# Performance work log

Measured on AMD Instinct MI355X. Metric: run time of the kernel, lower is better.

The kernel has to match this reference:

```python
import jax, jax.numpy as jnp
import numpy as np

D = 256        # embedding_dim
N = 32768      # number of latent vectors (tokens)
K = 8192       # num_embeddings (codebook size)


def setup_inputs() -> dict:
    key = jax.random.key(0)
    k1, k2 = jax.random.split(key)
    z_e = jax.random.normal(k1, (D, N), dtype=jnp.float32)
    embeddings = jax.random.normal(k2, (K, D), dtype=jnp.float32)
    return {"z_e": z_e, "embeddings": embeddings}


def reference(z_e, embeddings):
    # z_e: (D, N), embeddings: (K, D)
    z = z_e.T  # (N, D)
    # squared euclidean distance via expansion ||z||^2 - 2 z.e + ||e||^2
    # (mathematically identical to sum((emb - z)**2, -1), avoids (N,K,D) temp)
    z_sq = jnp.sum(z * z, axis=1, keepdims=True)            # (N, 1)
    e_sq = jnp.sum(embeddings * embeddings, axis=1)         # (K,)
    dist = z_sq - 2.0 * (z @ embeddings.T) + e_sq[None, :]  # (N, K)
    indices = jnp.argmin(dist, axis=-1)                     # (N,)
    z_q = embeddings[indices].T                             # (D, N)
    return z_q, indices
```

## Files before the change

kernel.cpp:

```cpp
#include <hip/hip_runtime.h>

#define D_DIM 256
#define N_TOK 32768
#define K_CB  8192
#define TAU   0.12f
#define ZC_CAP 4096
#define SLABS 32
#define SLABW 256

typedef float    f32x16 __attribute__((ext_vector_type(16)));
typedef float    f32x4  __attribute__((ext_vector_type(4)));
typedef _Float16 f16x8  __attribute__((ext_vector_type(8)));

#define OFF_ESQ   0
#define OFF_CNT   32768
#define OFF_GDONE 33024
#define OFF_LIST  35072
#define OFF_FIXB  166144
#define OFF_EHT   524288
#define OFF_ZC    (OFF_EHT + 4194304)
#define OFF_PBV   (OFF_ZC + 4194304)
#define OFF_PSC   (OFF_PBV + 262144)
#define OFF_PBK   (OFF_PSC + 262144)
#define MAXGRP    512
#define WS_NEED   ((size_t)(OFF_PBK + 262144))

#define SMEM_MAIN 65536

__global__ __launch_bounds__(256) void eprep_kernel(const float* __restrict__ e,
                                                    short* __restrict__ eht,
                                                    float* __restrict__ esq,
                                                    int* __restrict__ cnt,
                                                    int* __restrict__ gdone) {
  __shared__ float ps[4 * 64];
  const int tid = threadIdx.x;
  const int kk = tid & 63, cc = tid >> 6;
  const int k = blockIdx.x * 64 + kk;
  if (blockIdx.x == 0) {
    if (tid == 0) *cnt = 0;
    if (tid < 256) { gdone[tid] = 0; gdone[tid + 256] = 0; }
  }
  _Float16* ef = (_Float16*)eht;
  float ss = 0.f;
  #pragma unroll
  for (int c2 = 0; c2 < 8; ++c2) {
    const int c = cc * 8 + c2;
    f32x4 v0 = *(const f32x4*)(e + (size_t)k * D_DIM + c * 8);
    f32x4 v1 = *(const f32x4*)(e + (size_t)k * D_DIM + c * 8 + 4);
    float v[8] = {v0[0], v0[1], v0[2], v0[3], v1[0], v1[1], v1[2], v1[3]};
    f16x8 hv;
    #pragma unroll
    for (int i = 0; i < 8; ++i) {
      ss += v[i] * v[i];
      hv[i] = (_Float16)v[i];
    }
    *(f16x8*)(ef + ((size_t)c * K_CB + k) * 8) = hv;
  }
  ps[cc * 64 + kk] = ss;
  __syncthreads();
  if (tid < 64)
    esq[blockIdx.x * 64 + tid] = ps[tid] + ps[64 + tid] + ps[128 + tid] + ps[192 + tid];
}

__global__ __launch_bounds__(512, 4) void vq_main_kernel(
    const float* __restrict__ z, const float* __restrict__ esq_g,
    const short* __restrict__ eht,
    float* __restrict__ pbv, float* __restrict__ psc, int* __restrict__ pbk) {
  extern __shared__ char smem[];
  _Float16* zs = (_Float16*)smem;

  const int tid  = threadIdx.x;
  const int w    = tid >> 6;
  const int lane = tid & 63;
  const int half = lane >> 5;
  const int l31  = lane & 31;
  const int tg   = blockIdx.x >> 1;
  const int kh   = blockIdx.x & 1;
  const int n0   = tg * 128;
  const _Float16* ef = (const _Float16*)eht;

  {
    const int t  = tid & 127;
    const int cb = (tid >> 7) * 8;
    #pragma unroll
    for (int cc = 0; cc < 8; ++cc) {
      const int c = cb + cc;
      f16x8 hv;
      #pragma unroll
      for (int i = 0; i < 8; ++i)
        hv[i] = (_Float16)(-2.0f * z[(size_t)(c * 8 + i) * N_TOK + n0 + t]);
      *(f16x8*)(zs + ((size_t)c * 128 + t) * 8) = hv;
    }
  }
  __syncthreads();

  float bestv[4] = {3.4e38f, 3.4e38f, 3.4e38f, 3.4e38f};
  float secv[4]  = {3.4e38f, 3.4e38f, 3.4e38f, 3.4e38f};
  int   bestk[4] = {0, 0, 0, 0};

  const int kbase = kh * (K_CB / 2);
  for (int k0 = 0; k0 < K_CB / 2; k0 += 256) {
    const int kb = kbase + k0 + w * 32;

    f32x16 acc[4];
    {
      const int qb = kb + 4 * half;
      #pragma unroll
      for (int g = 0; g < 4; ++g) {
        f32x4 q = *(const f32x4*)(esq_g + qb + 8 * g);
        #pragma unroll
        for (int r = 0; r < 4; ++r) {
          const float qv = q[r];
          #pragma unroll
          for (int j = 0; j < 4; ++j) acc[j][g * 4 + r] = qv;
        }
      }
    }

    #pragma unroll 1
    for (int dc = 0; dc < 16; ++dc) {
      f16x8 a, b[4];
      a = *(const f16x8*)(ef + ((size_t)(2 * dc + half) * K_CB + kb + l31) * 8);
      const int zb = ((2 * dc + half) * 128 + l31) * 8;
      #pragma unroll
      for (int j = 0; j < 4; ++j)
        b[j] = *(const f16x8*)(zs + zb + j * 32 * 8);
      #pragma unroll
      for (int j = 0; j < 4; ++j)
        acc[j] = __builtin_amdgcn_mfma_f32_32x32x16_f16(a, b[j], acc[j], 0, 0, 0);
    }

    {
      const int base = kb + 4 * half;
      #pragma unroll
      for (int g = 0; g < 4; ++g) {
        #pragma unroll
        for (int r = 0; r < 4; ++r) {
          const int reg = g * 4 + r;
          const int kglob = base + 8 * g + r;
          #pragma unroll
          for (int j = 0; j < 4; ++j) {
            const float s = acc[j][reg];
            if (s < bestv[j]) { secv[j] = bestv[j]; bestv[j] = s; bestk[j] = kglob; }
            else if (s < secv[j]) secv[j] = s;
          }
        }
      }
    }
  }

  __syncthreads();
  float* pv  = (float*)(smem);
  int*   pk  = (int*)  (smem + 8192);
  float* ps2 = (float*)(smem + 16384);
  const int slot = w * 2 + half;
  #pragma unroll
  for (int j = 0; j < 4; ++j) {
    const int t = j * 32 + l31;
    pv [slot * 128 + t] = bestv[j];
    pk [slot * 128 + t] = bestk[j];
    ps2[slot * 128 + t] = secv[j];
  }
  __syncthreads();
  if (tid < 128) {
    const int t = tid;
    float bv = pv[t]; int bk = pk[t]; float sc = ps2[t];
    #pragma unroll
    for (int s2 = 1; s2 < 16; ++s2) {
      float v = pv[s2 * 128 + t]; int k2 = pk[s2 * 128 + t]; float s3 = ps2[s2 * 128 + t];
      if (v < bv || (v == bv && k2 < bk)) { sc = fminf(bv, s3); bv = v; bk = k2; }
      else                                { sc = fminf(sc, v); }
    }
    const size_t o = ((size_t)kh * 256 + tg) * 128 + t;
    pbv[o] = bv; psc[o] = sc; pbk[o] = bk;
  }
}

__global__ __launch_bounds__(256) void vq_merge_kernel(
    const float* __restrict__ z, const float* __restrict__ e,
    const float* __restrict__ pbv, const float* __restrict__ psc,
    const int* __restrict__ pbk,
    float* __restrict__ out, int* __restrict__ cnt, int* __restrict__ list,
    unsigned long long* __restrict__ fixb, float* __restrict__ zc) {
  __shared__ int fin[128], slo[128];
  const int tid = threadIdx.x;
  const int g = blockIdx.x;
  const int n0 = g * 128;
  if (tid < 128) {
    const size_t o0 = ((size_t)g) * 128 + tid;
    const size_t o1 = ((size_t)256 + g) * 128 + tid;
    const float bv0 = pbv[o0], bv1 = pbv[o1];
    const float sc0 = psc[o0], sc1 = psc[o1];
    const int   bk0 = pbk[o0], bk1 = pbk[o1];
    float bv, sc; int bk;
    if (bv0 <= bv1) { bv = bv0; bk = bk0; sc = fminf(sc0, bv1); }
    else            { bv = bv1; bk = bk1; sc = fminf(sc1, bv0); }
    fin[tid] = bk;
    int sl = -1;
    const int n = n0 + tid;
    out[(size_t)D_DIM * N_TOK + n] = (float)bk;
    if (sc - bv < TAU) {
      int p = atomicAdd(cnt, 1);
      list[p] = n;
      fixb[n] = 0xFFFFFFFFFFFFFFFFULL;
      if (p < ZC_CAP) sl = p;
    }
    slo[tid] = sl;
  }
  __syncthreads();
  for (int tt = 0; tt < 128; ++tt) {
    const int p = slo[tt];
    if (p >= 0)
      zc[(size_t)p * 256 + tid] = z[(size_t)tid * N_TOK + n0 + tt];
  }
  {
    const int t = tid & 127, d0 = tid >> 7;
    const int kk = fin[t];
    const f32x4* row = (const f32x4*)(e + (size_t)kk * D_DIM) + d0 * 32;
    #pragma unroll 4
    for (int q = 0; q < 32; ++q) {
      f32x4 v = row[q];
      const int d = d0 * 128 + q * 4;
      out[(size_t)(d + 0) * N_TOK + n0 + t] = v[0];
      out[(size_t)(d + 1) * N_TOK + n0 + t] = v[1];
      out[(size_t)(d + 2) * N_TOK + n0 + t] = v[2];
      out[(size_t)(d + 3) * N_TOK + n0 + t] = v[3];
    }
  }
}

__global__ __launch_bounds__(256) void rescan_kernel(
    const float* __restrict__ z, const float* __restrict__ zc,
    const float* __restrict__ e,
    const float* __restrict__ esq, const int* __restrict__ cnt,
    const int* __restrict__ list, unsigned long long* __restrict__ fixb,
    int* __restrict__ gdone, float* __restrict__ out) {
  __shared__ float zs[D_DIM * 64];
  __shared__ unsigned long long red[16 * 64];
  __shared__ int fk[64], fn[64], lastflag;
  const int tid = threadIdx.x;
  const int c = *(volatile const int*)cnt;
  if (c == 0) return;
  int groups = (c + 63) >> 6;
  if (groups > MAXGRP) groups = MAXGRP;
  const int items = groups * SLABS;
  const int tx = tid & 15, ty = tid >> 4;

  for (int it = blockIdx.x; it < items; it += gridDim.x) {
    const int g = it / SLABS;
    const int slab = (it % SLABS) * SLABW;
    __syncthreads();
    if (g < (ZC_CAP >> 6)) {
      const int t = tid & 63, seg = tid >> 6;
      const int idx = g * 64 + t;
      const float* src = zc + (size_t)(idx < c ? idx : c - 1) * 256 + seg * 64;
      #pragma unroll
      for (int r = 0; r < 16; ++r) {
        f32x4 v = *(const f32x4*)(src + r * 4);
        const int d = seg * 64 + r * 4;
        zs[(d + 0) * 64 + t] = v[0];
        zs[(d + 1) * 64 + t] = v[1];
        zs[(d + 2) * 64 + t] = v[2];
        zs[(d + 3) * 64 + t] = v[3];
      }
    } else {
      const int t = tid & 63, dq = tid >> 6;
      const int idx = g * 64 + t;
      const int n = list[idx < c ? idx : c - 1];
      #pragma unroll 4
      for (int dd = 0; dd < 64; ++dd) {
        const int d = dq * 64 + dd;
        zs[d * 64 + t] = z[(size_t)d * N_TOK + n];
      }
    }
    __syncthreads();

    unsigned long long lmin[4] = {~0ULL, ~0ULL, ~0ULL, ~0ULL};
    #pragma unroll
    for (int k0 = 0; k0 < SLABW; k0 += 64) {
      const f32x4* er[4]; float eqv[4];
      #pragma unroll
      for (int j = 0; j < 4; ++j) {
        int k = slab + k0 + ty + 16 * j;
        er[j] = (const f32x4*)(e + (size_t)k * D_DIM);
        eqv[j] = esq[k];
      }
      float acc[4][4];
      #pragma unroll
      for (int i = 0; i < 4; ++i)
        #pragma unroll
        for (int j = 0; j < 4; ++j) acc[i][j] = 0.f;
      #pragma unroll 4
      for (int d4 = 0; d4 < D_DIM / 4; ++d4) {
        f32x4 ev[4];
        #pragma unroll
        for (int j = 0; j < 4; ++j) ev[j] = er[j][d4];
        #pragma unroll
        for (int dd = 0; dd < 4; ++dd) {
          float zv[4];
          #pragma unroll
          for (int i = 0; i < 4; ++i) zv[i] = zs[(d4 * 4 + dd) * 64 + tx + 16 * i];
          #pragma unroll
          for (int i = 0; i < 4; ++i)
            #pragma unroll
            for (int j = 0; j < 4; ++j) acc[i][j] += zv[i] * ev[j][dd];
        }
      }
      #pragma unroll
      for (int j = 0; j < 4; ++j) {
        const int k = slab + k0 + ty + 16 * j;
        #pragma unroll
        for (int i = 0; i < 4; ++i) {
          float s = eqv[j] - 2.0f * acc[i][j] + 1024.0f;
          unsigned long long p =
              ((unsigned long long)__float_as_uint(s) << 32) | (unsigned)k;
          lmin[i] = (p < lmin[i]) ? p : lmin[i];
        }
      }
    }
    #pragma unroll
    for (int i = 0; i < 4; ++i) red[ty * 64 + tx + 16 * i] = lmin[i];
    __syncthreads();
    if (tid < 64) {
      unsigned long long m = red[tid];
      #pragma unroll
      for (int t = 1; t < 16; ++t) {
        unsigned long long v = red[t * 64 + tid];
        m = (v < m) ? v : m;
      }
      const int idx = g * 64 + tid;
      const int n = list[idx < c ? idx : c - 1];
      atomicMin(&fixb[n], m);
    }
    __threadfence();
    __syncthreads();
    if (tid == 0) lastflag = (atomicAdd(&gdone[g], 1) == SLABS - 1) ? 1 : 0;
    __syncthreads();
    if (lastflag) {
      if (tid < 64) {
        const int idx = g * 64 + tid;
        int kres = -1, n = -1;
        if (idx < c) {
          n = list[idx];
          unsigned long long mv = atomicMin(&fixb[n], 0xFFFFFFFFFFFFFFFFULL);
          kres = (int)(unsigned)(mv & 0xFFFFFFFFu);
          out[(size_t)D_DIM * N_TOK + n] = (float)kres;
        }
        fk[tid] = kres; fn[tid] = n;
      }
      __syncthreads();
      {
        const int t = tid & 63, dq = tid >> 6;
        const int kres = fk[t];
        if (kres >= 0) {
          const int n = fn[t];
          const float* row = e + (size_t)kres * D_DIM;
          #pragma unroll 4
          for (int dd = 0; dd < 64; ++dd) {
            const int d = dq * 64 + dd;
            out[(size_t)d * N_TOK + n] = row[d];
          }
        }
      }
    }
  }
}

__global__ __launch_bounds__(256) void esq_kernel(const float* __restrict__ e,
                                                  float* __restrict__ esq) {
  const int wave = threadIdx.x >> 6, lane = threadIdx.x & 63;
  const int k = blockIdx.x * 4 + wave;
  const float4* row = (const float4*)(e + (size_t)k * D_DIM);
  float4 v = row[lane];
  float s = v.x*v.x + v.y*v.y + v.z*v.z + v.w*v.w;
  #pragma unroll
  for (int off = 32; off > 0; off >>= 1) s += __shfl_down(s, off, 64);
  if (lane == 0) esq[k] = s;
}

__global__ __launch_bounds__(256) void vq_kernel(const float* __restrict__ z,
                                                 const float* __restrict__ e,
                                                 const float* __restrict__ esq,
                                                 float* __restrict__ out) {
  __shared__ float zs[D_DIM][64];
  const int tid = threadIdx.x, tx = tid & 15, ty = tid >> 4;
  const int n0 = blockIdx.x * 64;
  {
    const int c = tid & 63, d0 = tid >> 6;
    #pragma unroll 4
    for (int d = d0; d < D_DIM; d += 4) zs[d][c] = z[(size_t)d * N_TOK + n0 + c];
  }
  __syncthreads();
  float bestv[4] = {3.4e38f,3.4e38f,3.4e38f,3.4e38f};
  int   besti[4] = {0,0,0,0};
  for (int k0 = 0; k0 < K_CB; k0 += 64) {
    const float4* er[4]; float eqv[4];
    #pragma unroll
    for (int j = 0; j < 4; ++j) {
      int k = k0 + ty + 16 * j;
      er[j] = (const float4*)(e + (size_t)k * D_DIM);
      eqv[j] = esq[k];
    }
    float acc[4][4];
    #pragma unroll
    for (int i = 0; i < 4; ++i)
      #pragma unroll
      for (int j = 0; j < 4; ++j) acc[i][j] = 0.f;
    #pragma unroll 4
    for (int d4 = 0; d4 < D_DIM/4; ++d4) {
      float4 ev[4];
      #pragma unroll
      for (int j = 0; j < 4; ++j) ev[j] = er[j][d4];
      #pragma unroll
      for (int dd = 0; dd < 4; ++dd) {
        float zv[4];
        #pragma unroll
        for (int i = 0; i < 4; ++i) zv[i] = zs[d4*4+dd][tx + 16*i];
        #pragma unroll
        for (int i = 0; i < 4; ++i)
          #pragma unroll
          for (int j = 0; j < 4; ++j) acc[i][j] += zv[i] * ((const float*)&ev[j])[dd];
      }
    }
    #pragma unroll
    for (int j = 0; j < 4; ++j) {
      int k = k0 + ty + 16 * j;
      #pragma unroll
      for (int i = 0; i < 4; ++i) {
        float s = eqv[j] - 2.0f * acc[i][j];
        if (s < bestv[i]) { bestv[i] = s; besti[i] = k; }
      }
    }
  }
  __syncthreads();
  float* lds = &zs[0][0];
  float* vred = lds; int* ired = (int*)lds + 1024; int* fin = (int*)lds + 2048;
  #pragma unroll
  for (int i = 0; i < 4; ++i) {
    int l = tx + 16 * i;
    vred[ty * 64 + l] = bestv[i]; ired[ty * 64 + l] = besti[i];
  }
  __syncthreads();
  if (tid < 64) {
    float bv = vred[tid]; int bi = ired[tid];
    #pragma unroll
    for (int t = 1; t < 16; ++t) {
      float v = vred[t*64+tid]; int ix = ired[t*64+tid];
      if (v < bv || (v == bv && ix < bi)) { bv = v; bi = ix; }
    }
    fin[tid] = bi;
    out[(size_t)D_DIM * N_TOK + n0 + tid] = (float)bi;
  }
  __syncthreads();
  {
    const int l = tid & 63, d0 = tid >> 6;
    const int kk = fin[l];
    const float* row = e + (size_t)kk * D_DIM;
    #pragma unroll 4
    for (int d = d0; d < D_DIM; d += 4) out[(size_t)d * N_TOK + n0 + l] = row[d];
  }
}

extern "C" void kernel_launch(void* const* d_in, const int* in_sizes, int n_in,
                              void* d_out, int out_size, void* d_ws, size_t ws_size,
                              hipStream_t stream) {
  const float* z = (const float*)d_in[0];
  const float* e = (const float*)d_in[1];
  float* out = (float*)d_out;
  char* ws = (char*)d_ws;

  if (ws_size >= WS_NEED) {
    float* esq = (float*)(ws + OFF_ESQ);
    int* cnt = (int*)(ws + OFF_CNT);
    int* gdone = (int*)(ws + OFF_GDONE);
    int* list = (int*)(ws + OFF_LIST);
    unsigned long long* fixb = (unsigned long long*)(ws + OFF_FIXB);
    short* eht = (short*)(ws + OFF_EHT);
    float* zc = (float*)(ws + OFF_ZC);
    float* pbv = (float*)(ws + OFF_PBV);
    float* psc = (float*)(ws + OFF_PSC);
    int*   pbk = (int*)  (ws + OFF_PBK);

    (void)hipFuncSetAttribute((const void*)vq_main_kernel,
                              hipFuncAttributeMaxDynamicSharedMemorySize, SMEM_MAIN);

    eprep_kernel<<<128, 256, 0, stream>>>(e, eht, esq, cnt, gdone);
    vq_main_kernel<<<512, 512, SMEM_MAIN, stream>>>(z, esq, eht, pbv, psc, pbk);
    vq_merge_kernel<<<256, 256, 0, stream>>>(z, e, pbv, psc, pbk,
                                             out, cnt, list, fixb, zc);
    rescan_kernel<<<512, 256, 0, stream>>>(z, zc, e, esq, cnt, list, fixb, gdone, out);
  } else {
    float* esq = (float*)(ws);
    esq_kernel<<<K_CB / 4, 256, 0, stream>>>(e, esq);
    vq_kernel<<<N_TOK / 64, 256, 0, stream>>>(z, e, esq, out);
  }
}
```

Measured before the change: 347.4 us.

## Fuse K-halves and merge into single 1024-thread VQ main kernel

Instead of splitting the codebook into two halves across paired blocks and merging their partial best, second-best and index results in a separate kernel, each 1024-thread block now scans the full codebook for its 128 tokens. The block does the 32-slot reduction, ambiguity flagging and the codebook gather/output write itself. This removes one launch and the global round-trip of partial results, and the inner MFMA loop is unrolled by 2. In exchange the grid halves to 256 blocks of 1024 threads, which may reduce occupancy and latency hiding on the CUs, and the gather and copy epilogue now runs inside the large block.

```diff
diff --git a/kernel.cpp b/kernel.cpp
--- a/kernel.cpp
+++ b/kernel.cpp
@@ -19,11 +19,8 @@
 #define OFF_FIXB  166144
 #define OFF_EHT   524288
 #define OFF_ZC    (OFF_EHT + 4194304)
-#define OFF_PBV   (OFF_ZC + 4194304)
-#define OFF_PSC   (OFF_PBV + 262144)
-#define OFF_PBK   (OFF_PSC + 262144)
 #define MAXGRP    512
-#define WS_NEED   ((size_t)(OFF_PBK + 262144))
+#define WS_NEED   ((size_t)(OFF_ZC + 4194304))
 
 #define SMEM_MAIN 65536
 
@@ -62,28 +59,30 @@
     esq[blockIdx.x * 64 + tid] = ps[tid] + ps[64 + tid] + ps[128 + tid] + ps[192 + tid];
 }
 
-__global__ __launch_bounds__(512, 4) void vq_main_kernel(
-    const float* __restrict__ z, const float* __restrict__ esq_g,
+__global__ __launch_bounds__(1024, 4) void vq_main_kernel(
+    const float* __restrict__ z, const float* __restrict__ e,
+    const float* __restrict__ esq_g,
     const short* __restrict__ eht,
-    float* __restrict__ pbv, float* __restrict__ psc, int* __restrict__ pbk) {
+    float* __restrict__ out,
+    int* __restrict__ cnt, int* __restrict__ list,
+    unsigned long long* __restrict__ fixb, float* __restrict__ zc) {
   extern __shared__ char smem[];
   _Float16* zs = (_Float16*)smem;
+  __shared__ int fin[128], slo[128];
 
   const int tid  = threadIdx.x;
   const int w    = tid >> 6;
   const int lane = tid & 63;
   const int half = lane >> 5;
   const int l31  = lane & 31;
-  const int tg   = blockIdx.x >> 1;
-  const int kh   = blockIdx.x & 1;
-  const int n0   = tg * 128;
+  const int n0   = blockIdx.x * 128;
   const _Float16* ef = (const _Float16*)eht;
 
   {
     const int t  = tid & 127;
-    const int cb = (tid >> 7) * 8;
-    #pragma unroll
-    for (int cc = 0; cc < 8; ++cc) {
+    const int cb = (tid >> 7) * 4;
+    #pragma unroll
+    for (int cc = 0; cc < 4; ++cc) {
       const int c = cb + cc;
       f16x8 hv;
       #pragma unroll
@@ -98,9 +97,8 @@
   float secv[4]  = {3.4e38f, 3.4e38f, 3.4e38f, 3.4e38f};
   int   bestk[4] = {0, 0, 0, 0};
 
-  const int kbase = kh * (K_CB / 2);
-  for (int k0 = 0; k0 < K_CB / 2; k0 += 256) {
-    const int kb = kbase + k0 + w * 32;
+  for (int k0 = 0; k0 < K_CB; k0 += 512) {
+    const int kb = k0 + w * 32;
 
     f32x16 acc[4];
     {
@@ -117,7 +115,7 @@
       }
     }
 
-    #pragma unroll 1
+    #pragma unroll 2
     for (int dc = 0; dc < 16; ++dc) {
       f16x8 a, b[4];
       a = *(const f16x8*)(ef + ((size_t)(2 * dc + half) * K_CB + kb + l31) * 8);
@@ -151,8 +149,8 @@
 
   __syncthreads();
   float* pv  = (float*)(smem);
-  int*   pk  = (int*)  (smem + 8192);
-  float* ps2 = (float*)(smem + 16384);
+  int*   pk  = (int*)  (smem + 16384);
+  float* ps2 = (float*)(smem + 32768);
   const int slot = w * 2 + half;
   #pragma unroll
   for (int j = 0; j < 4; ++j) {
@@ -166,38 +164,14 @@
     const int t = tid;
     float bv = pv[t]; int bk = pk[t]; float sc = ps2[t];
     #pragma unroll
-    for (int s2 = 1; s2 < 16; ++s2) {
+    for (int s2 = 1; s2 < 32; ++s2) {
       float v = pv[s2 * 128 + t]; int k2 = pk[s2 * 128 + t]; float s3 = ps2[s2 * 128 + t];
       if (v < bv || (v == bv && k2 < bk)) { sc = fminf(bv, s3); bv = v; bk = k2; }
       else                                { sc = fminf(sc, v); }
     }
-    const size_t o = ((size_t)kh * 256 + tg) * 128 + t;
-    pbv[o] = bv; psc[o] = sc; pbk[o] = bk;
-  }
-}
-
-__global__ __launch_bounds__(256) void vq_merge_kernel(
-    const float* __restrict__ z, const float* __restrict__ e,
-    const float* __restrict__ pbv, const float* __restrict__ psc,
-    const int* __restrict__ pbk,
-    float* __restrict__ out, int* __restrict__ cnt, int* __restrict__ list,
-    unsigned long long* __restrict__ fixb, float* __restrict__ zc) {
-  __shared__ int fin[128], slo[128];
-  const int tid = threadIdx.x;
-  const int g = blockIdx.x;
-  const int n0 = g * 128;
-  if (tid < 128) {
-    const size_t o0 = ((size_t)g) * 128 + tid;
-    const size_t o1 = ((size_t)256 + g) * 128 + tid;
-    const float bv0 = pbv[o0], bv1 = pbv[o1];
-    const float sc0 = psc[o0], sc1 = psc[o1];
-    const int   bk0 = pbk[o0], bk1 = pbk[o1];
-    float bv, sc; int bk;
-    if (bv0 <= bv1) { bv = bv0; bk = bk0; sc = fminf(sc0, bv1); }
-    else            { bv = bv1; bk = bk1; sc = fminf(sc1, bv0); }
-    fin[tid] = bk;
+    fin[t] = bk;
     int sl = -1;
-    const int n = n0 + tid;
+    const int n = n0 + t;
     out[(size_t)D_DIM * N_TOK + n] = (float)bk;
     if (sc - bv < TAU) {
       int p = atomicAdd(cnt, 1);
@@ -205,22 +179,24 @@
       fixb[n] = 0xFFFFFFFFFFFFFFFFULL;
       if (p < ZC_CAP) sl = p;
     }
-    slo[tid] = sl;
-  }
-  __syncthreads();
+    slo[t] = sl;
+  }
+  __syncthreads();
+
   for (int tt = 0; tt < 128; ++tt) {
     const int p = slo[tt];
-    if (p >= 0)
+    if (p >= 0 && tid < 256)
       zc[(size_t)p * 256 + tid] = z[(size_t)tid * N_TOK + n0 + tt];
   }
+
   {
     const int t = tid & 127, d0 = tid >> 7;
     const int kk = fin[t];
-    const f32x4* row = (const f32x4*)(e + (size_t)kk * D_DIM) + d0 * 32;
+    const f32x4* row = (const f32x4*)(e + (size_t)kk * D_DIM) + d0 * 8;
     #pragma unroll 4
-    for (int q = 0; q < 32; ++q) {
+    for (int q = 0; q < 8; ++q) {
       f32x4 v = row[q];
-      const int d = d0 * 128 + q * 4;
+      const int d = d0 * 32 + q * 4;
       out[(size_t)(d + 0) * N_TOK + n0 + t] = v[0];
       out[(size_t)(d + 1) * N_TOK + n0 + t] = v[1];
       out[(size_t)(d + 2) * N_TOK + n0 + t] = v[2];
@@ -477,17 +453,13 @@
     unsigned long long* fixb = (unsigned long long*)(ws + OFF_FIXB);
     short* eht = (short*)(ws + OFF_EHT);
     float* zc = (float*)(ws + OFF_ZC);
-    float* pbv = (float*)(ws + OFF_PBV);
-    float* psc = (float*)(ws + OFF_PSC);
-    int*   pbk = (int*)  (ws + OFF_PBK);
 
     (void)hipFuncSetAttribute((const void*)vq_main_kernel,
                               hipFuncAttributeMaxDynamicSharedMemorySize, SMEM_MAIN);
 
     eprep_kernel<<<128, 256, 0, stream>>>(e, eht, esq, cnt, gdone);
-    vq_main_kernel<<<512, 512, SMEM_MAIN, stream>>>(z, esq, eht, pbv, psc, pbk);
-    vq_merge_kernel<<<256, 256, 0, stream>>>(z, e, pbv, psc, pbk,
-                                             out, cnt, list, fixb, zc);
+    vq_main_kernel<<<256, 1024, SMEM_MAIN, stream>>>(z, e, esq, eht,
+                                                     out, cnt, list, fixb, zc);
     rescan_kernel<<<512, 256, 0, stream>>>(z, zc, e, esq, cnt, list, fixb, gdone, out);
   } else {
     float* esq = (float*)(ws);
```

Result: faster. 340.5 us (-2.0%).
